# Optimization experiments

Measured on AMD Instinct MI355X. Metric: run time of the kernel, lower is better.

Reference implementation:

```python
import jax, jax.numpy as jnp
import numpy as np

D_MODEL = 1024


def bitlinear(x, weight):
    # ternary quantization with straight-through estimator; forward value is w_q*scale
    scale = jnp.clip(jnp.mean(jnp.abs(weight), axis=1, keepdims=True), 1e-5, None)
    w_q = jnp.clip(jnp.round(weight / scale), -1.0, 1.0)
    w = weight + jax.lax.stop_gradient(w_q * scale - weight)
    return x @ w.T


def rmsnorm(x, w, eps=1e-6):
    return x * jax.lax.rsqrt(jnp.mean(x * x, axis=-1, keepdims=True) + eps) * w


def setup_inputs() -> dict:
    key = jax.random.key(0)
    ks = jax.random.split(key, 6)
    D = D_MODEL
    std = np.sqrt(2.0 / D)  # kaiming_normal fan_out
    return {
        "x": jax.random.normal(ks[0], (4, 4096, D), dtype=jnp.float32),
        "Wr": jax.random.normal(ks[1], (D, D), dtype=jnp.float32) * std,
        "Wk": jax.random.normal(ks[2], (D, D), dtype=jnp.float32) * std,
        "Wv": jax.random.normal(ks[3], (D, D), dtype=jnp.float32) * std,
        "Wo": jax.random.normal(ks[4], (D, D), dtype=jnp.float32) * std,
        "decay": jnp.ones((D,), dtype=jnp.float32) * 0.99,
        "ln_w": jnp.ones((D,), dtype=jnp.float32),
    }


def reference(x, Wr, Wk, Wv, Wo, decay, ln_w):
    B, T, D = x.shape
    r = jax.nn.sigmoid(bitlinear(x, Wr))
    k = bitlinear(x, Wk)
    v = bitlinear(x, Wv)
    dec = jax.nn.sigmoid(decay)                              # [D]
    kv = k * v                                               # [B,T,D]
    positions = jnp.arange(T, dtype=x.dtype)                 # [T]
    log_decay = jnp.log(jnp.clip(dec, 1e-7, None))           # [D]
    scale = jnp.exp(positions[:, None] * log_decay[None, :])  # [T,D]
    scaled = kv / jnp.clip(scale, 1e-10, None)[None]         # [B,T,D]
    cum = jnp.cumsum(scaled, axis=1)                         # [B,T,D]
    state = cum * scale[None]                                # [B,T,D]
    return bitlinear(rmsnorm(r * state, ln_w), Wo)
```

## Files before the change

kernel.cpp:

```cpp
#include <hip/hip_runtime.h>

typedef unsigned short u16;
typedef __attribute__((ext_vector_type(8))) short bf16x8;
typedef __attribute__((ext_vector_type(4))) float f32x4;
typedef __attribute__((ext_vector_type(4))) int   i32x4;
typedef __attribute__((ext_vector_type(4))) unsigned short u16x4;

#define DM 1024

__device__ __forceinline__ float bf2f(u16 u){
  union { unsigned int i; float f; } v; v.i = ((unsigned int)u)<<16; return v.f;
}
__device__ __forceinline__ u16 f2bf(float f){
  unsigned int x = __float_as_uint(f);
  return (u16)((x + 0x7FFFu + ((x>>16)&1u)) >> 16);
}

__global__ __launch_bounds__(256)
void init_pack(const float* __restrict__ W0, const float* __restrict__ W1,
               const float* __restrict__ W2, const float* __restrict__ W3,
               const float* __restrict__ x,
               u16* __restrict__ wq, signed char* __restrict__ wq8,
               float* __restrict__ wsc, u16* __restrict__ xb)
{
  if (blockIdx.x >= 1024){
    const int i = ((blockIdx.x-1024)*256 + threadIdx.x)*4;
    float4 v = *(const float4*)&x[i];
    u16x4 o; o[0]=f2bf(v.x); o[1]=f2bf(v.y); o[2]=f2bf(v.z); o[3]=f2bf(v.w);
    *(u16x4*)&xb[i] = o;
    return;
  }
  const int gr   = blockIdx.x*4 + (threadIdx.x>>6);
  const int lane = threadIdx.x & 63;
  const float* W; int row;
  if (gr < 1024)      { W = W0; row = gr; }
  else if (gr < 3072) { row = (gr-1024)>>1; W = (gr&1) ? W2 : W1; }
  else                { W = W3; row = gr-3072; }
  const float* wr = W + (size_t)row*DM;
  float4 v[4]; float s = 0.f;
  #pragma unroll
  for (int c=0;c<4;c++){
    v[c] = *(const float4*)&wr[c*256 + lane*4];
    s += fabsf(v[c].x)+fabsf(v[c].y)+fabsf(v[c].z)+fabsf(v[c].w);
  }
  #pragma unroll
  for (int off=32; off; off>>=1) s += __shfl_down(s, off);
  s = __shfl(s, 0);
  const float scale = fmaxf(s*(1.f/1024.f), 1e-5f);
  if (lane==0) wsc[gr] = scale;
  if (gr < 3072){
    u16* wo = wq + (size_t)gr*DM;
    #pragma unroll
    for (int c=0;c<4;c++){
      u16x4 q;
      q[0] = f2bf(fminf(fmaxf(rintf(v[c].x/scale),-1.f),1.f));
      q[1] = f2bf(fminf(fmaxf(rintf(v[c].y/scale),-1.f),1.f));
      q[2] = f2bf(fminf(fmaxf(rintf(v[c].z/scale),-1.f),1.f));
      q[3] = f2bf(fminf(fmaxf(rintf(v[c].w/scale),-1.f),1.f));
      *(u16x4*)&wo[c*256 + lane*4] = q;
    }
  } else {
    signed char* wo = wq8 + (size_t)(gr-3072)*DM;
    #pragma unroll
    for (int c=0;c<4;c++){
      const int q0 = (int)rintf(fminf(fmaxf(v[c].x/scale,-1.f),1.f));
      const int q1 = (int)rintf(fminf(fmaxf(v[c].y/scale,-1.f),1.f));
      const int q2 = (int)rintf(fminf(fmaxf(v[c].z/scale,-1.f),1.f));
      const int q3 = (int)rintf(fminf(fmaxf(v[c].w/scale,-1.f),1.f));
      const unsigned int p = (q0&0xFF) | ((q1&0xFF)<<8) | ((q2&0xFF)<<16) | ((unsigned)(q3&0xFF)<<24);
      *(unsigned int*)&wo[c*256 + lane*4] = p;
    }
  }
}

#define RD(base, off) (*(const bf16x8*)((const char*)(base) + (off)))

__global__ __launch_bounds__(256, 4)
void gemm_rkv(const u16* __restrict__ Ag, const u16* __restrict__ Bq,
              const float* __restrict__ bscale,
              u16* __restrict__ o_r, u16* __restrict__ o_kv)
{
  __shared__ u16 sA[128*64];
  __shared__ u16 sB[128*64];
  const int tid = threadIdx.x, wave = tid>>6, lane = tid&63;
  const int lr = lane&15, lg = lane>>4;
  const int wm = wave>>1, wn = wave&1;
  const int bm0 = blockIdx.x*128, bn0 = blockIdx.y*128;
  constexpr int nt = 16;

  const int r8   = lane>>3;
  const int scol = ((lane&7)<<4) ^ (r8<<4);
  const size_t aoff = (size_t)(bm0 + wave*8 + r8)*2048 + scol;
  const size_t boff = (size_t)(bn0 + wave*8 + r8)*2048 + scol;
  const int ldst = wave*1024;

  const int S = (lr&7)<<4;
  const int koff0 = ((lg<<4)     ) ^ S;
  const int koff1 = (64 + (lg<<4)) ^ S;
  const int arow = (wm*64 + lr)*128;
  const int brow = (wn*64 + lr)*128;

  f32x4 acc[4][4];
  #pragma unroll
  for (int i=0;i<4;i++)
    #pragma unroll
    for (int j=0;j<4;j++) acc[i][j] = (f32x4){0.f,0.f,0.f,0.f};

  for (int t=0; t<nt; ++t){
    #pragma unroll
    for (int q=0;q<4;q++){
      __builtin_amdgcn_global_load_lds(
        (const __attribute__((address_space(1))) void*)((const char*)Ag + aoff + q*65536 + (size_t)t*128),
        (__attribute__((address_space(3))) void*)((char*)sA + ldst + q*4096), 16, 0, 0);
      __builtin_amdgcn_global_load_lds(
        (const __attribute__((address_space(1))) void*)((const char*)Bq + boff + q*65536 + (size_t)t*128),
        (__attribute__((address_space(3))) void*)((char*)sB + ldst + q*4096), 16, 0, 0);
    }
    __syncthreads();
    {
      bf16x8 a[4], b[4];
      #pragma unroll
      for (int m=0;m<4;m++) a[m] = RD(sA, arow + m*2048 + koff0);
      #pragma unroll
      for (int n=0;n<4;n++) b[n] = RD(sB, brow + n*2048 + koff0);
      #pragma unroll
      for (int m=0;m<4;m++)
        #pragma unroll
        for (int n=0;n<4;n++)
          acc[m][n] = __builtin_amdgcn_mfma_f32_16x16x32_bf16(a[m], b[n], acc[m][n], 0,0,0);
      #pragma unroll
      for (int m=0;m<4;m++) a[m] = RD(sA, arow + m*2048 + koff1);
      #pragma unroll
      for (int n=0;n<4;n++) b[n] = RD(sB, brow + n*2048 + koff1);
      #pragma unroll
      for (int m=0;m<4;m++)
        #pragma unroll
        for (int n=0;n<4;n++)
          acc[m][n] = __builtin_amdgcn_mfma_f32_16x16x32_bf16(a[m], b[n], acc[m][n], 0,0,0);
    }
    __syncthreads();
  }

  #pragma unroll
  for (int mi=0; mi<4; ++mi){
    #pragma unroll
    for (int ni=0; ni<4; ++ni){
      const int col = bn0 + wn*64 + ni*16 + lr;
      const float sc = bscale[col];
      const int rowb = bm0 + wm*64 + mi*16 + lg*4;
      const f32x4 a = acc[mi][ni];
      if (bn0 < 1024){
        #pragma unroll
        for (int r2=0;r2<4;r2++){
          const float val = a[r2]*sc;
          o_r[(size_t)(rowb+r2)*DM + col] = f2bf(1.f/(1.f+expf(-val)));
        }
      } else {
        const int dv = (col - 1024) >> 1;
        #pragma unroll
        for (int r2=0;r2<4;r2++){
          const float val = a[r2]*sc;
          const float pr  = val * __shfl_xor(val, 1);
          if (!(lr & 1))
            o_kv[(size_t)(rowb+r2)*DM + dv] = f2bf(pr);
        }
      }
    }
  }
}

#define RD8(base, off) (*(const i32x4*)((const char*)(base) + (off)))

__global__ __launch_bounds__(256, 4)
void gemm_o8(const signed char* __restrict__ Ag, const signed char* __restrict__ Bq,
             const float* __restrict__ bscale, const float* __restrict__ sxr,
             float* __restrict__ o_f)
{
  __shared__ signed char sA[128*128];
  __shared__ signed char sB[128*128];
  const int tid = threadIdx.x, wave = tid>>6, lane = tid&63;
  const int lr = lane&15, lg = lane>>4;
  const int wm = wave>>1, wn = wave&1;
  const int bm0 = blockIdx.x*128, bn0 = blockIdx.y*128;
  constexpr int nt = 8;

  const int r8   = lane>>3;
  const int scol = ((lane&7)<<4) ^ (r8<<4);
  const size_t aoff = (size_t)(bm0 + wave*8 + r8)*1024 + scol;
  const size_t boff = (size_t)(bn0 + wave*8 + r8)*1024 + scol;
  const int ldst = wave*1024;

  const int S = (lr&7)<<4;
  const int koff0 = ((lg<<4)     ) ^ S;
  const int koff1 = (64 + (lg<<4)) ^ S;
  const int arow = (wm*64 + lr)*128;
  const int brow = (wn*64 + lr)*128;

  i32x4 acc[4][4];
  #pragma unroll
  for (int i=0;i<4;i++)
    #pragma unroll
    for (int j=0;j<4;j++) acc[i][j] = (i32x4){0,0,0,0};

  for (int t=0; t<nt; ++t){
    #pragma unroll
    for (int q=0;q<4;q++){
      __builtin_amdgcn_global_load_lds(
        (const __attribute__((address_space(1))) void*)((const char*)Ag + aoff + q*32768 + (size_t)t*128),
        (__attribute__((address_space(3))) void*)((char*)sA + ldst + q*4096), 16, 0, 0);
      __builtin_amdgcn_global_load_lds(
        (const __attribute__((address_space(1))) void*)((const char*)Bq + boff + q*32768 + (size_t)t*128),
        (__attribute__((address_space(3))) void*)((char*)sB + ldst + q*4096), 16, 0, 0);
    }
    __syncthreads();
    {
      i32x4 a[4], b[4];
      #pragma unroll
      for (int m=0;m<4;m++) a[m] = RD8(sA, arow + m*2048 + koff0);
      #pragma unroll
      for (int n=0;n<4;n++) b[n] = RD8(sB, brow + n*2048 + koff0);
      #pragma unroll
      for (int m=0;m<4;m++)
        #pragma unroll
        for (int n=0;n<4;n++)
          acc[m][n] = __builtin_amdgcn_mfma_i32_16x16x64_i8(a[m], b[n], acc[m][n], 0,0,0);
      #pragma unroll
      for (int m=0;m<4;m++) a[m] = RD8(sA, arow + m*2048 + koff1);
      #pragma unroll
      for (int n=0;n<4;n++) b[n] = RD8(sB, brow + n*2048 + koff1);
      #pragma unroll
      for (int m=0;m<4;m++)
        #pragma unroll
        for (int n=0;n<4;n++)
          acc[m][n] = __builtin_amdgcn_mfma_i32_16x16x64_i8(a[m], b[n], acc[m][n], 0,0,0);
    }
    __syncthreads();
  }

  #pragma unroll
  for (int mi=0; mi<4; ++mi){
    const int rowb = bm0 + wm*64 + mi*16 + lg*4;
    float sx[4];
    #pragma unroll
    for (int r2=0;r2<4;r2++) sx[r2] = sxr[rowb+r2];
    #pragma unroll
    for (int ni=0; ni<4; ++ni){
      const int col = bn0 + wn*64 + ni*16 + lr;
      const float sc = bscale[col];
      const i32x4 a = acc[mi][ni];
      #pragma unroll
      for (int r2=0;r2<4;r2++)
        o_f[(size_t)(rowb+r2)*DM + col] = (float)a[r2] * sx[r2] * sc;
    }
  }
}

__global__ __launch_bounds__(256)
void kv_phase1(const u16* __restrict__ kv, const float* __restrict__ decay,
               float* __restrict__ part)
{
  const int c = blockIdx.x & 127, b = blockIdx.x >> 7;
  const int d0 = threadIdx.x*4;
  float rc[4], E1i[4]; f32x4 sum = {0.f,0.f,0.f,0.f};
  #pragma unroll
  for (int j=0;j<4;j++){
    const float dec = 1.f/(1.f+expf(-decay[d0+j]));
    const float ld  = logf(fmaxf(dec, 1e-7f));
    E1i[j] = expf(-ld);
    rc[j]  = expf(-(float)(c*32)*ld);
  }
  for (int t=c*32; t<c*32+32; ++t){
    const size_t base = ((size_t)(b*4096 + t))*DM + d0;
    const u16x4 p4 = *(const u16x4*)&kv[base];
    #pragma unroll
    for (int j=0;j<4;j++){
      sum[j] += bf2f(p4[j]) * fminf(rc[j], 1e10f);
      rc[j] *= E1i[j];
    }
  }
  *(f32x4*)&part[((size_t)(b*128+c))*DM + d0] = sum;
}

__global__ void chunk_prefix(float* __restrict__ part){
  const int g = blockIdx.x*256 + threadIdx.x;
  const int b = g >> 10, d = g & 1023;
  float run = 0.f;
  for (int c8=0; c8<128; c8+=8){
    float v[8];
    #pragma unroll
    for (int i=0;i<8;i++)
      v[i] = part[((size_t)(b*128+c8+i))*DM + d];
    #pragma unroll
    for (int i=0;i<8;i++){
      const float tmp = v[i];
      part[((size_t)(b*128+c8+i))*DM + d] = run;
      run += tmp;
    }
  }
}

__global__ __launch_bounds__(256)
void scan_norm(const u16* __restrict__ kv, const u16* __restrict__ rbuf,
               const float* __restrict__ part, const float* __restrict__ decay,
               const float* __restrict__ lnw, signed char* __restrict__ yn8,
               float* __restrict__ sxr)
{
  const int c = blockIdx.x & 127, b = blockIdx.x >> 7;
  const int tid = threadIdx.x, lane = tid&63, wave = tid>>6;
  const int d0 = tid*4;
  __shared__ float redS[2][4];
  __shared__ float redM[2][4];
  f32x4 run = *(const f32x4*)&part[((size_t)(b*128+c))*DM + d0];
  float lw[4], e[4], E1[4], rc[4], E1i[4];
  #pragma unroll
  for (int j=0;j<4;j++){
    const float dec = 1.f/(1.f+expf(-decay[d0+j]));
    const float ld  = logf(fmaxf(dec, 1e-7f));
    lw[j]  = lnw[d0+j];
    E1[j]  = expf(ld);
    E1i[j] = expf(-ld);
    e[j]   = expf((float)(c*32)*ld);
    rc[j]  = expf(-(float)(c*32)*ld);
  }
  for (int t=c*32; t<c*32+32; ++t){
    const size_t base = ((size_t)(b*4096+t))*DM + d0;
    const u16x4 p4 = *(const u16x4*)&kv[base];
    const u16x4 r4 = *(const u16x4*)&rbuf[base];
    float yl[4]; float ss = 0.f, mx = 0.f;
    #pragma unroll
    for (int j=0;j<4;j++){
      run[j] += bf2f(p4[j]) * fminf(rc[j], 1e10f);
      const float st = run[j]*e[j];
      const float y = bf2f(r4[j])*st;
      ss += y*y;
      yl[j] = y*lw[j];
      mx = fmaxf(mx, fabsf(yl[j]));
      rc[j] *= E1i[j];
      e[j]  *= E1[j];
    }
    #pragma unroll
    for (int off=32; off; off>>=1){
      ss += __shfl_down(ss, off);
      mx  = fmaxf(mx, __shfl_down(mx, off));
    }
    if (lane==0){ redS[t&1][wave] = ss; redM[t&1][wave] = mx; }
    __builtin_amdgcn_s_barrier();
    const float tot = (redS[t&1][0]+redS[t&1][1])+(redS[t&1][2]+redS[t&1][3]);
    const float m1  = fmaxf(fmaxf(redM[t&1][0],redM[t&1][1]),
                            fmaxf(redM[t&1][2],redM[t&1][3]));
    const float rs  = 1.f/sqrtf(tot*(1.f/1024.f) + 1e-6f);
    const float m1s = fmaxf(m1, 1e-30f);
    const float qk  = 127.f/m1s;
    if (tid==0) sxr[b*4096+t] = m1s*rs*(1.f/127.f);
    unsigned int p = 0;
    #pragma unroll
    for (int j=0;j<4;j++){
      int q = (int)rintf(yl[j]*qk);
      q = q>127?127:(q<-127?-127:q);
      p |= ((unsigned)(q&0xFF)) << (8*j);
    }
    *(unsigned int*)&yn8[base] = p;
  }
}

extern "C" void kernel_launch(void* const* d_in, const int* in_sizes, int n_in,
                              void* d_out, int out_size, void* d_ws, size_t ws_size,
                              hipStream_t stream)
{
  (void)in_sizes; (void)n_in; (void)out_size; (void)ws_size;
  const float* x    = (const float*)d_in[0];
  const float* Wr   = (const float*)d_in[1];
  const float* Wk   = (const float*)d_in[2];
  const float* Wv   = (const float*)d_in[3];
  const float* Wo   = (const float*)d_in[4];
  const float* dec  = (const float*)d_in[5];
  const float* lnw  = (const float*)d_in[6];

  char* ws = (char*)d_ws;
  u16*         wq    = (u16*)(ws + 0);
  signed char* wq8   = (signed char*)(ws + 6291456);
  float*       wsc   = (float*)(ws + 7340032);
  u16*         rbuf  = (u16*)(ws + 7356416);
  u16*         kvbuf = (u16*)(ws + 40910848);
  float*       part  = (float*)(ws + 74465280);
  u16*         xb    = (u16*)(ws + 76562432);
  signed char* yn8   = (signed char*)(ws + 110116864);
  float*       sxr   = (float*)(ws + 126894080);

  init_pack<<<17408, 256, 0, stream>>>(Wr, Wk, Wv, Wo, x, wq, wq8, wsc, xb);
  gemm_rkv<<<dim3(128,24), 256, 0, stream>>>(xb, wq, wsc, rbuf, kvbuf);
  kv_phase1<<<512, 256, 0, stream>>>(kvbuf, dec, part);
  chunk_prefix<<<16, 256, 0, stream>>>(part);
  scan_norm<<<512, 256, 0, stream>>>(kvbuf, rbuf, part, dec, lnw, yn8, sxr);
  gemm_o8<<<dim3(128,8), 256, 0, stream>>>(yn8, wq8, wsc + 3072, sxr, (float*)d_out);
}
```

Baseline: 202.5 us.

## Fuse chunked decay scan phases into one kernel with atomic inter-block sync

Merges the per-chunk partial-sum kernel, the chunk prefix kernel and the scan/normalize kernel into a single launch. Each block keeps its 32 kv rows in registers so kv is read once instead of twice. Cross-block dependencies are handled by an atomic counter per batch, a serial prefix done by chunk-0 blocks, and a release flag that the other blocks spin on. This removes two kernel launches and a second kv read, at the cost of spin-waiting, higher register pressure, and reliance on all 512 blocks being co-resident to avoid deadlock.

```diff
diff --git a/kernel.cpp b/kernel.cpp
--- a/kernel.cpp
+++ b/kernel.cpp
@@ -256,62 +256,19 @@
 }
 
 __global__ __launch_bounds__(256)
-void kv_phase1(const u16* __restrict__ kv, const float* __restrict__ decay,
-               float* __restrict__ part)
-{
-  const int c = blockIdx.x & 127, b = blockIdx.x >> 7;
-  const int d0 = threadIdx.x*4;
-  float rc[4], E1i[4]; f32x4 sum = {0.f,0.f,0.f,0.f};
-  #pragma unroll
-  for (int j=0;j<4;j++){
-    const float dec = 1.f/(1.f+expf(-decay[d0+j]));
-    const float ld  = logf(fmaxf(dec, 1e-7f));
-    E1i[j] = expf(-ld);
-    rc[j]  = expf(-(float)(c*32)*ld);
-  }
-  for (int t=c*32; t<c*32+32; ++t){
-    const size_t base = ((size_t)(b*4096 + t))*DM + d0;
-    const u16x4 p4 = *(const u16x4*)&kv[base];
-    #pragma unroll
-    for (int j=0;j<4;j++){
-      sum[j] += bf2f(p4[j]) * fminf(rc[j], 1e10f);
-      rc[j] *= E1i[j];
-    }
-  }
-  *(f32x4*)&part[((size_t)(b*128+c))*DM + d0] = sum;
-}
-
-__global__ void chunk_prefix(float* __restrict__ part){
-  const int g = blockIdx.x*256 + threadIdx.x;
-  const int b = g >> 10, d = g & 1023;
-  float run = 0.f;
-  for (int c8=0; c8<128; c8+=8){
-    float v[8];
-    #pragma unroll
-    for (int i=0;i<8;i++)
-      v[i] = part[((size_t)(b*128+c8+i))*DM + d];
-    #pragma unroll
-    for (int i=0;i<8;i++){
-      const float tmp = v[i];
-      part[((size_t)(b*128+c8+i))*DM + d] = run;
-      run += tmp;
-    }
-  }
-}
-
-__global__ __launch_bounds__(256)
-void scan_norm(const u16* __restrict__ kv, const u16* __restrict__ rbuf,
-               const float* __restrict__ part, const float* __restrict__ decay,
-               const float* __restrict__ lnw, signed char* __restrict__ yn8,
-               float* __restrict__ sxr)
+void scan_fused(const u16* __restrict__ kv, const u16* __restrict__ rbuf,
+                float* __restrict__ part, const float* __restrict__ decay,
+                const float* __restrict__ lnw, signed char* __restrict__ yn8,
+                float* __restrict__ sxr,
+                unsigned int* __restrict__ cnt, unsigned int* __restrict__ flag)
 {
   const int c = blockIdx.x & 127, b = blockIdx.x >> 7;
   const int tid = threadIdx.x, lane = tid&63, wave = tid>>6;
   const int d0 = tid*4;
   __shared__ float redS[2][4];
   __shared__ float redM[2][4];
-  f32x4 run = *(const f32x4*)&part[((size_t)(b*128+c))*DM + d0];
-  float lw[4], e[4], E1[4], rc[4], E1i[4];
+
+  float lw[4], E1[4], E1i[4], e0[4], rc0[4];
   #pragma unroll
   for (int j=0;j<4;j++){
     const float dec = 1.f/(1.f+expf(-decay[d0+j]));
@@ -319,17 +276,75 @@
     lw[j]  = lnw[d0+j];
     E1[j]  = expf(ld);
     E1i[j] = expf(-ld);
-    e[j]   = expf((float)(c*32)*ld);
-    rc[j]  = expf(-(float)(c*32)*ld);
-  }
-  for (int t=c*32; t<c*32+32; ++t){
+    e0[j]  = expf((float)(c*32)*ld);
+    rc0[j] = expf(-(float)(c*32)*ld);
+  }
+
+  u16x4 kvr[32];
+  {
+    f32x4 sum = {0.f,0.f,0.f,0.f};
+    float rca[4] = {rc0[0],rc0[1],rc0[2],rc0[3]};
+    #pragma unroll
+    for (int s=0;s<32;s++){
+      kvr[s] = *(const u16x4*)&kv[((size_t)(b*4096 + c*32 + s))*DM + d0];
+      #pragma unroll
+      for (int j=0;j<4;j++){
+        sum[j] += bf2f(kvr[s][j]) * fminf(rca[j], 1e10f);
+        rca[j] *= E1i[j];
+      }
+    }
+    *(f32x4*)&part[((size_t)(b*128+c))*DM + d0] = sum;
+  }
+  __threadfence();
+  __syncthreads();
+  if (tid==0)
+    __hip_atomic_fetch_add(&cnt[b], 1u, __ATOMIC_ACQ_REL, __HIP_MEMORY_SCOPE_AGENT);
+
+  if (c == 0){
+    if (tid==0){
+      while (__hip_atomic_load(&cnt[b], __ATOMIC_ACQUIRE, __HIP_MEMORY_SCOPE_AGENT) < 128u)
+        __builtin_amdgcn_s_sleep(8);
+    }
+    __syncthreads();
+    __threadfence();
+    f32x4 run2 = {0.f,0.f,0.f,0.f};
+    for (int c8=0; c8<128; c8+=8){
+      f32x4 v[8];
+      #pragma unroll
+      for (int i=0;i<8;i++)
+        v[i] = *(const f32x4*)&part[((size_t)(b*128+c8+i))*DM + d0];
+      #pragma unroll
+      for (int i=0;i<8;i++){
+        const f32x4 tmp = v[i];
+        *(f32x4*)&part[((size_t)(b*128+c8+i))*DM + d0] = run2;
+        run2 += tmp;
+      }
+    }
+    __threadfence();
+    __syncthreads();
+    if (tid==0)
+      __hip_atomic_store(&flag[b], 1u, __ATOMIC_RELEASE, __HIP_MEMORY_SCOPE_AGENT);
+  }
+
+  if (tid==0){
+    while (__hip_atomic_load(&flag[b], __ATOMIC_ACQUIRE, __HIP_MEMORY_SCOPE_AGENT) == 0u)
+      __builtin_amdgcn_s_sleep(16);
+  }
+  __syncthreads();
+  __threadfence();
+
+  f32x4 run = *(const f32x4*)&part[((size_t)(b*128+c))*DM + d0];
+  float e[4]  = {e0[0], e0[1], e0[2], e0[3]};
+  float rc[4] = {rc0[0],rc0[1],rc0[2],rc0[3]};
+  #pragma unroll
+  for (int s=0;s<32;s++){
+    const int t = c*32 + s;
     const size_t base = ((size_t)(b*4096+t))*DM + d0;
-    const u16x4 p4 = *(const u16x4*)&kv[base];
     const u16x4 r4 = *(const u16x4*)&rbuf[base];
     float yl[4]; float ss = 0.f, mx = 0.f;
     #pragma unroll
     for (int j=0;j<4;j++){
-      run[j] += bf2f(p4[j]) * fminf(rc[j], 1e10f);
+      run[j] += bf2f(kvr[s][j]) * fminf(rc[j], 1e10f);
       const float st = run[j]*e[j];
       const float y = bf2f(r4[j])*st;
       ss += y*y;
@@ -343,11 +358,11 @@
       ss += __shfl_down(ss, off);
       mx  = fmaxf(mx, __shfl_down(mx, off));
     }
-    if (lane==0){ redS[t&1][wave] = ss; redM[t&1][wave] = mx; }
-    __builtin_amdgcn_s_barrier();
-    const float tot = (redS[t&1][0]+redS[t&1][1])+(redS[t&1][2]+redS[t&1][3]);
-    const float m1  = fmaxf(fmaxf(redM[t&1][0],redM[t&1][1]),
-                            fmaxf(redM[t&1][2],redM[t&1][3]));
+    if (lane==0){ redS[s&1][wave] = ss; redM[s&1][wave] = mx; }
+    __syncthreads();
+    const float tot = (redS[s&1][0]+redS[s&1][1])+(redS[s&1][2]+redS[s&1][3]);
+    const float m1  = fmaxf(fmaxf(redM[s&1][0],redM[s&1][1]),
+                            fmaxf(redM[s&1][2],redM[s&1][3]));
     const float rs  = 1.f/sqrtf(tot*(1.f/1024.f) + 1e-6f);
     const float m1s = fmaxf(m1, 1e-30f);
     const float qk  = 127.f/m1s;
@@ -377,20 +392,21 @@
   const float* lnw  = (const float*)d_in[6];
 
   char* ws = (char*)d_ws;
-  u16*         wq    = (u16*)(ws + 0);
-  signed char* wq8   = (signed char*)(ws + 6291456);
-  float*       wsc   = (float*)(ws + 7340032);
-  u16*         rbuf  = (u16*)(ws + 7356416);
-  u16*         kvbuf = (u16*)(ws + 40910848);
-  float*       part  = (float*)(ws + 74465280);
-  u16*         xb    = (u16*)(ws + 76562432);
-  signed char* yn8   = (signed char*)(ws + 110116864);
-  float*       sxr   = (float*)(ws + 126894080);
-
+  u16*          wq    = (u16*)(ws + 0);
+  signed char*  wq8   = (signed char*)(ws + 6291456);
+  float*        wsc   = (float*)(ws + 7340032);
+  u16*          rbuf  = (u16*)(ws + 7356416);
+  u16*          kvbuf = (u16*)(ws + 40910848);
+  float*        part  = (float*)(ws + 74465280);
+  u16*          xb    = (u16*)(ws + 76562432);
+  signed char*  yn8   = (signed char*)(ws + 110116864);
+  float*        sxr   = (float*)(ws + 126894080);
+  unsigned int* cnt   = (unsigned int*)(ws + 126959616);
+  unsigned int* flag  = (unsigned int*)(ws + 126959648);
+
+  hipMemsetAsync(ws + 126959616, 0, 64, stream);
   init_pack<<<17408, 256, 0, stream>>>(Wr, Wk, Wv, Wo, x, wq, wq8, wsc, xb);
   gemm_rkv<<<dim3(128,24), 256, 0, stream>>>(xb, wq, wsc, rbuf, kvbuf);
-  kv_phase1<<<512, 256, 0, stream>>>(kvbuf, dec, part);
-  chunk_prefix<<<16, 256, 0, stream>>>(part);
-  scan_norm<<<512, 256, 0, stream>>>(kvbuf, rbuf, part, dec, lnw, yn8, sxr);
+  scan_fused<<<512, 256, 0, stream>>>(kvbuf, rbuf, part, dec, lnw, yn8, sxr, cnt, flag);
   gemm_o8<<<dim3(128,8), 256, 0, stream>>>(yn8, wq8, wsc + 3072, sxr, (float*)d_out);
 }
```

After: 489.2 us. +141.6%, slower.
